# Kernel optimization log

Hardware: AMD Instinct MI355X
Metric: run time of the kernel (lower is better)

The kernel has to match this reference:

```python
import jax, jax.numpy as jnp
import numpy as np

N_NODES = 50000
N_EDGES = 800000
D = 128
N_RELS = 460  # 2 * num_rels
N_BASES = 32
SUBMAT = D // N_BASES  # 4
INV_TEMP = 0.1


def setup_inputs() -> dict:
    key = jax.random.key(0)
    ks = jax.random.split(key, 16)
    return {
        "h": jax.random.normal(ks[0], (N_NODES, D), jnp.float32),
        "first_prev": jax.random.normal(ks[1], (N_NODES, D), jnp.float32),
        "second_prev": jax.random.normal(ks[2], (N_NODES, D), jnp.float32),
        "time_diff": jax.random.uniform(ks[3], (N_NODES, 1), jnp.float32),
        "edge_src": jax.random.randint(ks[4], (N_EDGES,), 0, N_NODES, jnp.int32),
        "edge_dst": jax.random.randint(ks[5], (N_EDGES,), 0, N_NODES, jnp.int32),
        "edge_type": jax.random.randint(ks[6], (N_EDGES,), 0, N_RELS, jnp.int32),
        "edge_norm": jax.random.uniform(ks[7], (N_EDGES, 1), jnp.float32),
        "node_norm": jax.random.uniform(ks[8], (N_NODES, 1), jnp.float32),
        "W1": jax.random.normal(ks[9], (N_RELS, N_BASES * SUBMAT * SUBMAT), jnp.float32) * 0.05,
        "W2": jax.random.normal(ks[10], (N_RELS, N_BASES * SUBMAT * SUBMAT), jnp.float32) * 0.05,
        "loop_w1": jax.random.normal(ks[11], (D, D), jnp.float32) * 0.05,
        "loop_w2": jax.random.normal(ks[12], (D, D), jnp.float32) * 0.05,
        "time_w1": jax.random.normal(ks[13], (D, D), jnp.float32) * 0.05,
        "time_w2": jax.random.normal(ks[14], (D, D), jnp.float32) * 0.05,
    }


def _drgcn_layer(h, prev, time_diff, W, loop_w, time_w,
                 edge_src, edge_dst, edge_type, edge_norm, node_norm, activate):
    n = h.shape[0]
    # self-loop message (dropout is identity in eval)
    loop_msg = h @ loop_w                                     # [N, D]
    # block-diagonal per-edge message: gather relation blocks + batched small matmul
    w = W[edge_type].reshape(-1, N_BASES, SUBMAT, SUBMAT)     # [E, B, si, so]
    hs = h[edge_src].reshape(-1, N_BASES, SUBMAT)             # [E, B, si]
    msg = jnp.einsum('ebi,ebio->ebo', hs, w).reshape(-1, h.shape[1])  # [E, D]
    msg = msg * edge_norm                                     # per-edge norm
    agg = jax.ops.segment_sum(msg, edge_dst, num_segments=n)  # scatter-sum to dst
    agg = agg * node_norm                                     # apply_func node norm
    # time-decay residual + self-loop (bias=None in this config)
    out = agg + (prev @ time_w) * jnp.exp(-time_diff * INV_TEMP) + loop_msg
    if activate:
        out = jax.nn.relu(out)
    return out


def reference(h, first_prev, second_prev, time_diff,
              edge_src, edge_dst, edge_type, edge_norm, node_norm,
              W1, W2, loop_w1, loop_w2, time_w1, time_w2):
    h1 = _drgcn_layer(h, first_prev, time_diff, W1, loop_w1, time_w1,
                      edge_src, edge_dst, edge_type, edge_norm, node_norm, activate=False)
    h2 = _drgcn_layer(h1, second_prev, time_diff, W2, loop_w2, time_w2,
                      edge_src, edge_dst, edge_type, edge_norm, node_norm, activate=True)
    return (h1, h2)
```

## Files before the change

### kernel.cpp

```cpp
#include <hip/hip_runtime.h>

#define NN 50000
#define NE 800000
#define DD 128
#define NPAD 50176
#define NBLK_SCAN 196

typedef __attribute__((ext_vector_type(8))) short short8;
typedef __attribute__((ext_vector_type(4))) float f32x4;

static __device__ __forceinline__ float b2f(unsigned short u) {
    return __builtin_bit_cast(float, (unsigned)u << 16);
}
static __device__ __forceinline__ float b2f_lo(unsigned u) {
    return __builtin_bit_cast(float, u << 16);
}
static __device__ __forceinline__ float b2f_hi(unsigned u) {
    return __builtin_bit_cast(float, u & 0xffff0000u);
}
static __device__ __forceinline__ unsigned short f2b(float f) {
    unsigned u = __builtin_bit_cast(unsigned, f);
    u += 0x7FFFu + ((u >> 16) & 1u);
    return (unsigned short)(u >> 16);
}

__global__ __launch_bounds__(256) void k_hist(
    const int* __restrict__ edst, int* __restrict__ cnt)
{
    const int e = blockIdx.x * 256 + threadIdx.x;
    atomicAdd(&cnt[edst[e]], 1);
}

__global__ __launch_bounds__(256) void k_scan_a(
    const int* __restrict__ cnt, int* __restrict__ bsum)
{
    __shared__ int s[256];
    const int t = threadIdx.x;
    s[t] = cnt[blockIdx.x * 256 + t];
    __syncthreads();
    for (int d = 128; d > 0; d >>= 1) {
        if (t < d) s[t] += s[t + d];
        __syncthreads();
    }
    if (t == 0) bsum[blockIdx.x] = s[0];
}

__global__ __launch_bounds__(256) void k_scan_b(int* __restrict__ bsum)
{
    __shared__ int s[256];
    const int t = threadIdx.x;
    s[t] = (t < NBLK_SCAN) ? bsum[t] : 0;
    __syncthreads();
    for (int d = 1; d < 256; d <<= 1) {
        int v = (t >= d) ? s[t - d] : 0;
        __syncthreads();
        s[t] += v;
        __syncthreads();
    }
    bsum[t] = (t == 0) ? 0 : s[t - 1];
}

__global__ __launch_bounds__(256) void k_scan_c(
    const int* __restrict__ cnt, const int* __restrict__ bsum,
    int* __restrict__ off, int* __restrict__ cur)
{
    __shared__ int s[256];
    const int t = threadIdx.x;
    const int i = blockIdx.x * 256 + t;
    const int c = cnt[i];
    s[t] = c;
    __syncthreads();
    for (int d = 1; d < 256; d <<= 1) {
        int v = (t >= d) ? s[t - d] : 0;
        __syncthreads();
        s[t] += v;
        __syncthreads();
    }
    const int ex = bsum[blockIdx.x] + s[t] - c;
    off[i] = ex;
    cur[i] = ex;
}

__global__ __launch_bounds__(256) void k_scatter(
    const int* __restrict__ esrc, const int* __restrict__ edst,
    const int* __restrict__ etyp, const float* __restrict__ enorm,
    int* __restrict__ cur, int4* __restrict__ sedge)
{
    const int e = blockIdx.x * 256 + threadIdx.x;
    const int d = edst[e];
    const int pos = atomicAdd(&cur[d], 1);
    sedge[pos] = make_int4(esrc[e], etyp[e],
                           __builtin_bit_cast(int, enorm[e]), d);
}

__global__ __launch_bounds__(256) void conv_x(
    const float* __restrict__ x, const float* __restrict__ fprev,
    const float* __restrict__ sprev, const float* __restrict__ tdiff,
    unsigned short* __restrict__ X1, unsigned short* __restrict__ X2)
{
    const int idx = blockIdx.x * 256 + threadIdx.x;
    const int n = idx >> 7, j = idx & 127;
    const float d = __expf(-tdiff[n] * 0.1f);
    X1[(size_t)n * 256 + j]       = f2b(x[(size_t)n * 128 + j]);
    X1[(size_t)n * 256 + 128 + j] = f2b(fprev[(size_t)n * 128 + j] * d);
    X2[(size_t)n * 256 + 128 + j] = f2b(sprev[(size_t)n * 128 + j] * d);
}

__global__ __launch_bounds__(256) void k_wprep(
    const float* __restrict__ W1, const float* __restrict__ W2,
    unsigned short* __restrict__ W1b, unsigned short* __restrict__ W2b,
    const float* __restrict__ lw1, const float* __restrict__ tw1,
    const float* __restrict__ lw2, const float* __restrict__ tw2,
    unsigned short* __restrict__ Wp1, unsigned short* __restrict__ Wp2)
{
    const int gb = blockIdx.x;
    if (gb < 1840) {
        const int i = gb * 256 + threadIdx.x;
        if (i < 460 * 512) W1b[i] = f2b(W1[i]);
        else               W2b[i - 460 * 512] = f2b(W2[i - 460 * 512]);
    } else {
        const int g = (gb - 1840) * 256 + threadIdx.x;
        const int c = g & 4095;
        const float* lw = (g < 4096) ? lw1 : lw2;
        const float* tw = (g < 4096) ? tw1 : tw2;
        unsigned short* Wp = (g < 4096) ? Wp1 : Wp2;
        const int ct = c >> 9, ks = (c >> 6) & 7, lane = c & 63;
        const int col = ct * 16 + (lane & 15);
        unsigned short* o = Wp + (size_t)c * 8;
        #pragma unroll
        for (int i = 0; i < 8; ++i) {
            const int k = ks * 32 + (lane >> 4) * 8 + i;
            const float v = (k < 128) ? lw[(size_t)k * 128 + col]
                                      : tw[(size_t)(k - 128) * 128 + col];
            o[i] = f2b(v);
        }
    }
}

__device__ __forceinline__ void agg_edge(
    const unsigned short* __restrict__ x,
    const unsigned short* __restrict__ Wb,
    const int4* __restrict__ sedge, int i,
    int woff, int l, float4& acc)
{
    const int4 e = sedge[i];
    const int src = __builtin_amdgcn_readfirstlane(e.x);
    const int typ = __builtin_amdgcn_readfirstlane(e.y);
    const float nr = __builtin_bit_cast(float, __builtin_amdgcn_readfirstlane(e.z));
    const unsigned hw = ((const unsigned*)(x + (size_t)src * 256))[l];
    const uint4 wv = *(const uint4*)(Wb + (size_t)typ * 512 + woff);
    const float h0 = b2f_lo(hw) * nr;
    const float h1 = b2f_hi(hw) * nr;
    acc.x += h0 * b2f_lo(wv.x) + h1 * b2f_lo(wv.z);
    acc.y += h0 * b2f_hi(wv.x) + h1 * b2f_hi(wv.z);
    acc.z += h0 * b2f_lo(wv.y) + h1 * b2f_lo(wv.w);
    acc.w += h0 * b2f_hi(wv.y) + h1 * b2f_hi(wv.w);
}

__global__ __launch_bounds__(256) void k_agg2(
    const unsigned short* __restrict__ x,
    const int4*  __restrict__ sedge,
    const int*   __restrict__ off,
    const unsigned short* __restrict__ Wb,
    const float* __restrict__ nnorm,
    float*       __restrict__ agg)
{
    const int l = threadIdx.x & 63;
    const int n = blockIdx.x * 4 + (threadIdx.x >> 6);
    const int beg = off[n], end = off[n + 1];
    const int woff = (l >> 1) * 16 + (l & 1) * 8;

    float4 a0 = {0,0,0,0}, a1 = {0,0,0,0}, a2 = {0,0,0,0}, a3 = {0,0,0,0};

    int i = beg;
    for (; i + 4 <= end; i += 4) {
        agg_edge(x, Wb, sedge, i,     woff, l, a0);
        agg_edge(x, Wb, sedge, i + 1, woff, l, a1);
        agg_edge(x, Wb, sedge, i + 2, woff, l, a2);
        agg_edge(x, Wb, sedge, i + 3, woff, l, a3);
    }
    for (; i < end; ++i) agg_edge(x, Wb, sedge, i, woff, l, a0);

    float4 s;
    s.x = (a0.x + a1.x) + (a2.x + a3.x);
    s.y = (a0.y + a1.y) + (a2.y + a3.y);
    s.z = (a0.z + a1.z) + (a2.z + a3.z);
    s.w = (a0.w + a1.w) + (a2.w + a3.w);
    s.x += __shfl_xor(s.x, 1);
    s.y += __shfl_xor(s.y, 1);
    s.z += __shfl_xor(s.z, 1);
    s.w += __shfl_xor(s.w, 1);

    const float nn = nnorm[n];
    const float e0 = (l & 1) ? s.z : s.x;
    const float e1 = (l & 1) ? s.w : s.y;
    float2* outp = (float2*)(agg + (size_t)n * DD + (l >> 1) * 4 + (l & 1) * 2);
    *outp = make_float2(e0 * nn, e1 * nn);
}

template<int ACT, int WRITE_NEXT>
__global__ __launch_bounds__(256) void combine_mfma(
    const float* __restrict__ agg,
    const unsigned short* __restrict__ X,
    const unsigned short* __restrict__ Wp,
    float* __restrict__ out,
    unsigned short* __restrict__ Xnext)
{
    const int t = threadIdx.x;
    const int l = t & 63;
    const int w = t >> 6;
    const int wr = w >> 1, wc = w & 1;
    const int l15 = l & 15, lhi = l >> 4;
    const int rowbase = blockIdx.x * 64 + wr * 32;

    f32x4 acc[2][4] = {};

    const int ar0 = min(rowbase + l15, NN - 1);
    const int ar1 = min(rowbase + 16 + l15, NN - 1);
    const unsigned short* a0p = X + (size_t)ar0 * 256 + lhi * 8;
    const unsigned short* a1p = X + (size_t)ar1 * 256 + lhi * 8;
    const unsigned short* bp  = Wp + (size_t)(wc * 4) * 8 * 512 + (size_t)l * 8;

    #pragma unroll
    for (int ks = 0; ks < 8; ++ks) {
        const short8 a0 = *(const short8*)(a0p + ks * 32);
        const short8 a1 = *(const short8*)(a1p + ks * 32);
        #pragma unroll
        for (int ct = 0; ct < 4; ++ct) {
            const short8 b = *(const short8*)(bp + (size_t)(ct * 8 + ks) * 512);
            acc[0][ct] = __builtin_amdgcn_mfma_f32_16x16x32_bf16(a0, b, acc[0][ct], 0, 0, 0);
            acc[1][ct] = __builtin_amdgcn_mfma_f32_16x16x32_bf16(a1, b, acc[1][ct], 0, 0, 0);
        }
    }

    __shared__ float cs[64][132];
    #pragma unroll
    for (int rg = 0; rg < 2; ++rg)
        #pragma unroll
        for (int ct = 0; ct < 4; ++ct)
            #pragma unroll
            for (int q = 0; q < 4; ++q)
                cs[wr * 32 + rg * 16 + lhi * 4 + q][wc * 64 + ct * 16 + l15]
                    = acc[rg][ct][q];
    __syncthreads();

    const int r = t >> 2;
    const int s = t & 3;
    const int grow = blockIdx.x * 64 + r;
    if (grow < NN) {
        const float* aggr = agg + (size_t)grow * DD;
        float*       outr = out + (size_t)grow * DD;
        #pragma unroll
        for (int i = 0; i < 8; ++i) {
            const int c = s * 4 + i * 16;
            const float4 a  = *(const float4*)(aggr + c);
            const float4 cc = *(const float4*)&cs[r][c];
            float4 v = make_float4(a.x + cc.x, a.y + cc.y, a.z + cc.z, a.w + cc.w);
            if (ACT) {
                v.x = fmaxf(v.x, 0.f); v.y = fmaxf(v.y, 0.f);
                v.z = fmaxf(v.z, 0.f); v.w = fmaxf(v.w, 0.f);
            }
            *(float4*)(outr + c) = v;
            if (WRITE_NEXT) {
                ushort4 u;
                u.x = f2b(v.x); u.y = f2b(v.y); u.z = f2b(v.z); u.w = f2b(v.w);
                *(ushort4*)(Xnext + (size_t)grow * 256 + c) = u;
            }
        }
    }
}

__device__ __forceinline__ float pick4(float4 v, int o) {
    float a = (o & 1) ? v.y : v.x;
    float b = (o & 1) ? v.w : v.z;
    return (o & 2) ? b : a;
}

__global__ __launch_bounds__(256) void k_agg_t2(
    const float* __restrict__ x, const int4* __restrict__ sedge,
    const int* __restrict__ off, const float* __restrict__ W,
    float* __restrict__ agg)
{
    const int lane = threadIdx.x & 63;
    const int n    = blockIdx.x * 4 + (threadIdx.x >> 6);
    const int beg = off[n], end = off[n + 1];
    float4 acca = make_float4(0.f, 0.f, 0.f, 0.f);
    float4 accb = make_float4(0.f, 0.f, 0.f, 0.f);
    for (int i = beg; i < end; ++i) {
        const int4 e = sedge[i];
        const float nr = __builtin_bit_cast(float, e.z);
        const float* wr = W + (size_t)e.y * 512 + 4 * lane;
        const float4 wa = *(const float4*)wr;
        const float4 wb = *(const float4*)(wr + 256);
        const float* hr = x + (size_t)e.x * DD;
        const float ha = hr[lane] * nr;
        const float hb = hr[64 + lane] * nr;
        acca.x += ha * wa.x; acca.y += ha * wa.y; acca.z += ha * wa.z; acca.w += ha * wa.w;
        accb.x += hb * wb.x; accb.y += hb * wb.y; accb.z += hb * wb.z; accb.w += hb * wb.w;
    }
    #pragma unroll
    for (int d = 1; d <= 2; d <<= 1) {
        acca.x += __shfl_xor(acca.x, d); acca.y += __shfl_xor(acca.y, d);
        acca.z += __shfl_xor(acca.z, d); acca.w += __shfl_xor(acca.w, d);
        accb.x += __shfl_xor(accb.x, d); accb.y += __shfl_xor(accb.y, d);
        accb.z += __shfl_xor(accb.z, d); accb.w += __shfl_xor(accb.w, d);
    }
    const int o = lane & 3;
    agg[(size_t)n * DD + lane]      = pick4(acca, o);
    agg[(size_t)n * DD + 64 + lane] = pick4(accb, o);
}

__global__ __launch_bounds__(256) void edge_msg(
    const float* __restrict__ x, const int* __restrict__ esrc,
    const int* __restrict__ edst, const int* __restrict__ etyp,
    const float* __restrict__ enorm, const float* __restrict__ W,
    float* __restrict__ agg)
{
    const int t  = threadIdx.x;
    const int le = t >> 7;
    const int j  = t & 127;
    const int e  = blockIdx.x * 2 + le;
    __shared__ float sh[2][DD];
    sh[le][j] = x[(size_t)esrc[e] * DD + j];
    __syncthreads();
    const int b = j >> 2, o = j & 3;
    const float* wr = W + (size_t)etyp[e] * 512 + b * 16 + o;
    const float4 hv = *(const float4*)&sh[le][b * 4];
    float m = hv.x * wr[0] + hv.y * wr[4] + hv.z * wr[8] + hv.w * wr[12];
    m *= enorm[e];
    atomicAdd(&agg[(size_t)edst[e] * DD + j], m);
}

template<int ACT>
__global__ __launch_bounds__(256) void combine(
    float* __restrict__ out, const float* __restrict__ x,
    const float* __restrict__ prev, const float* __restrict__ tdiff,
    const float* __restrict__ nnorm, const float* __restrict__ lw,
    const float* __restrict__ tw)
{
    const int t = threadIdx.x;
    const int j = t & 127;
    const int r = t >> 7;
    const int base = blockIdx.x * 8;
    __shared__ float sh[8][DD];
    __shared__ float sp[8][DD];
    #pragma unroll
    for (int q = 0; q < 4; ++q) {
        const int m = q * 2 + r;
        const int n = base + m;
        const float decay = __expf(-tdiff[n] * 0.1f);
        sh[m][j] = x[(size_t)n * DD + j];
        sp[m][j] = prev[(size_t)n * DD + j] * decay;
    }
    __syncthreads();
    float acc[4] = {0.f, 0.f, 0.f, 0.f};
    for (int k = 0; k < DD; k += 4) {
        float wl[4], wt[4];
        #pragma unroll
        for (int kk = 0; kk < 4; ++kk) {
            wl[kk] = lw[(size_t)(k + kk) * DD + j];
            wt[kk] = tw[(size_t)(k + kk) * DD + j];
        }
        #pragma unroll
        for (int q = 0; q < 4; ++q) {
            const int m = q * 2 + r;
            const float4 a = *(const float4*)&sh[m][k];
            const float4 p = *(const float4*)&sp[m][k];
            acc[q] += a.x * wl[0] + a.y * wl[1] + a.z * wl[2] + a.w * wl[3]
                    + p.x * wt[0] + p.y * wt[1] + p.z * wt[2] + p.w * wt[3];
        }
    }
    #pragma unroll
    for (int q = 0; q < 4; ++q) {
        const int m = q * 2 + r;
        const int n = base + m;
        float v = out[(size_t)n * DD + j] * nnorm[n] + acc[q];
        if (ACT) v = fmaxf(v, 0.f);
        out[(size_t)n * DD + j] = v;
    }
}

extern "C" void kernel_launch(void* const* d_in, const int* in_sizes, int n_in,
                              void* d_out, int out_size, void* d_ws, size_t ws_size,
                              hipStream_t stream) {
    const float* h     = (const float*)d_in[0];
    const float* fprev = (const float*)d_in[1];
    const float* sprev = (const float*)d_in[2];
    const float* tdiff = (const float*)d_in[3];
    const int*   esrc  = (const int*)d_in[4];
    const int*   edst  = (const int*)d_in[5];
    const int*   etyp  = (const int*)d_in[6];
    const float* enorm = (const float*)d_in[7];
    const float* nnorm = (const float*)d_in[8];
    const float* W1    = (const float*)d_in[9];
    const float* W2    = (const float*)d_in[10];
    const float* lw1   = (const float*)d_in[11];
    const float* lw2   = (const float*)d_in[12];
    const float* tw1   = (const float*)d_in[13];
    const float* tw2   = (const float*)d_in[14];

    float* h1 = (float*)d_out;
    float* h2 = h1 + (size_t)NN * DD;
    const size_t layer_bytes = (size_t)NN * DD * sizeof(float);

    char* wsp = (char*)d_ws;
    int*   cnt   = (int*)wsp;  wsp += (size_t)NPAD * 4;
    int*   off   = (int*)wsp;  wsp += (size_t)NPAD * 4;
    int*   cur   = (int*)wsp;  wsp += (size_t)NPAD * 4;
    int*   bsum  = (int*)wsp;  wsp += 256 * 4;
    int4*  sedge = (int4*)wsp; wsp += (size_t)NE * 16;
    const size_t ws_sorted = (size_t)(wsp - (char*)d_ws);
    unsigned short* X1   = (unsigned short*)wsp; wsp += (size_t)NN * 256 * 2;
    unsigned short* X2   = (unsigned short*)wsp; wsp += (size_t)NN * 256 * 2;
    unsigned short* Wc1p = (unsigned short*)wsp; wsp += 4096 * 8 * 2;
    unsigned short* Wc2p = (unsigned short*)wsp; wsp += 4096 * 8 * 2;
    unsigned short* W1b  = (unsigned short*)wsp; wsp += (size_t)460 * 512 * 2;
    unsigned short* W2b  = (unsigned short*)wsp; wsp += (size_t)460 * 512 * 2;
    const size_t ws_full = (size_t)(wsp - (char*)d_ws);

    const int grid_mm = (NN + 63) / 64;

    if (ws_size >= ws_full) {
        hipMemsetAsync(cnt, 0, (size_t)NPAD * 4, stream);
        k_hist   <<<NE / 256, 256, 0, stream>>>(edst, cnt);
        k_scan_a <<<NBLK_SCAN, 256, 0, stream>>>(cnt, bsum);
        k_scan_b <<<1, 256, 0, stream>>>(bsum);
        k_scan_c <<<NBLK_SCAN, 256, 0, stream>>>(cnt, bsum, off, cur);
        k_scatter<<<NE / 256, 256, 0, stream>>>(esrc, edst, etyp, enorm, cur, sedge);
        conv_x <<<NN * DD / 256, 256, 0, stream>>>(h, fprev, sprev, tdiff, X1, X2);
        k_wprep<<<1872, 256, 0, stream>>>(W1, W2, W1b, W2b,
                                          lw1, tw1, lw2, tw2, Wc1p, Wc2p);
        k_agg2<<<NN / 4, 256, 0, stream>>>(X1, sedge, off, W1b, nnorm, h1);
        combine_mfma<0, 1><<<grid_mm, 256, 0, stream>>>(h1, X1, Wc1p, h1, X2);
        k_agg2<<<NN / 4, 256, 0, stream>>>(X2, sedge, off, W2b, nnorm, h2);
        combine_mfma<1, 0><<<grid_mm, 256, 0, stream>>>(h2, X2, Wc2p, h2, nullptr);
    } else if (ws_size >= ws_sorted) {
        hipMemsetAsync(cnt, 0, (size_t)NPAD * 4, stream);
        k_hist   <<<NE / 256, 256, 0, stream>>>(edst, cnt);
        k_scan_a <<<NBLK_SCAN, 256, 0, stream>>>(cnt, bsum);
        k_scan_b <<<1, 256, 0, stream>>>(bsum);
        k_scan_c <<<NBLK_SCAN, 256, 0, stream>>>(cnt, bsum, off, cur);
        k_scatter<<<NE / 256, 256, 0, stream>>>(esrc, edst, etyp, enorm, cur, sedge);
        k_agg_t2<<<NN / 4, 256, 0, stream>>>(h, sedge, off, W1, h1);
        combine<0><<<NN / 8, 256, 0, stream>>>(h1, h, fprev, tdiff, nnorm, lw1, tw1);
        k_agg_t2<<<NN / 4, 256, 0, stream>>>(h1, sedge, off, W2, h2);
        combine<1><<<NN / 8, 256, 0, stream>>>(h2, h1, sprev, tdiff, nnorm, lw2, tw2);
    } else {
        hipMemsetAsync(h1, 0, layer_bytes, stream);
        edge_msg<<<NE / 2, 256, 0, stream>>>(h, esrc, edst, etyp, enorm, W1, h1);
        combine<0><<<NN / 8, 256, 0, stream>>>(h1, h, fprev, tdiff, nnorm, lw1, tw1);
        hipMemsetAsync(h2, 0, layer_bytes, stream);
        edge_msg<<<NE / 2, 256, 0, stream>>>(h1, esrc, edst, etyp, enorm, W2, h2);
        combine<1><<<NN / 8, 256, 0, stream>>>(h2, h1, sprev, tdiff, nnorm, lw2, tw2);
    }
}
```

Baseline: 430.1 us.

## Fuse edge aggregation with MFMA combine into one kernel per layer

Merges the per-node gather/aggregation kernel and the MFMA self-loop/time-decay combine kernel into a single kernel per layer. Each block of 64 nodes first aggregates neighbour messages into shared memory, with each wave handling 16 nodes in sequence. It then adds that tile to the MFMA results before writing the output and the next layer's bf16 input. This removes the fp32 agg round trip through global memory and two kernel launches. In exchange the grid drops from 12500 small blocks to about 782, which reduces the number of waves available to hide the latency of the gathers.

```diff
diff --git a/kernel.cpp b/kernel.cpp
--- a/kernel.cpp
+++ b/kernel.cpp
@@ -9,9 +9,6 @@
 typedef __attribute__((ext_vector_type(8))) short short8;
 typedef __attribute__((ext_vector_type(4))) float f32x4;
 
-static __device__ __forceinline__ float b2f(unsigned short u) {
-    return __builtin_bit_cast(float, (unsigned)u << 16);
-}
 static __device__ __forceinline__ float b2f_lo(unsigned u) {
     return __builtin_bit_cast(float, u << 16);
 }
@@ -157,61 +154,65 @@
     acc.w += h0 * b2f_hi(wv.y) + h1 * b2f_hi(wv.w);
 }
 
-__global__ __launch_bounds__(256) void k_agg2(
-    const unsigned short* __restrict__ x,
+template<int ACT, int WRITE_NEXT>
+__global__ __launch_bounds__(256) void layer_fused(
+    const unsigned short* __restrict__ X,
     const int4*  __restrict__ sedge,
     const int*   __restrict__ off,
     const unsigned short* __restrict__ Wb,
+    const unsigned short* __restrict__ Wp,
     const float* __restrict__ nnorm,
-    float*       __restrict__ agg)
-{
-    const int l = threadIdx.x & 63;
-    const int n = blockIdx.x * 4 + (threadIdx.x >> 6);
-    const int beg = off[n], end = off[n + 1];
-    const int woff = (l >> 1) * 16 + (l & 1) * 8;
-
-    float4 a0 = {0,0,0,0}, a1 = {0,0,0,0}, a2 = {0,0,0,0}, a3 = {0,0,0,0};
-
-    int i = beg;
-    for (; i + 4 <= end; i += 4) {
-        agg_edge(x, Wb, sedge, i,     woff, l, a0);
-        agg_edge(x, Wb, sedge, i + 1, woff, l, a1);
-        agg_edge(x, Wb, sedge, i + 2, woff, l, a2);
-        agg_edge(x, Wb, sedge, i + 3, woff, l, a3);
-    }
-    for (; i < end; ++i) agg_edge(x, Wb, sedge, i, woff, l, a0);
-
-    float4 s;
-    s.x = (a0.x + a1.x) + (a2.x + a3.x);
-    s.y = (a0.y + a1.y) + (a2.y + a3.y);
-    s.z = (a0.z + a1.z) + (a2.z + a3.z);
-    s.w = (a0.w + a1.w) + (a2.w + a3.w);
-    s.x += __shfl_xor(s.x, 1);
-    s.y += __shfl_xor(s.y, 1);
-    s.z += __shfl_xor(s.z, 1);
-    s.w += __shfl_xor(s.w, 1);
-
-    const float nn = nnorm[n];
-    const float e0 = (l & 1) ? s.z : s.x;
-    const float e1 = (l & 1) ? s.w : s.y;
-    float2* outp = (float2*)(agg + (size_t)n * DD + (l >> 1) * 4 + (l & 1) * 2);
-    *outp = make_float2(e0 * nn, e1 * nn);
-}
-
-template<int ACT, int WRITE_NEXT>
-__global__ __launch_bounds__(256) void combine_mfma(
-    const float* __restrict__ agg,
-    const unsigned short* __restrict__ X,
-    const unsigned short* __restrict__ Wp,
     float* __restrict__ out,
     unsigned short* __restrict__ Xnext)
 {
     const int t = threadIdx.x;
     const int l = t & 63;
     const int w = t >> 6;
+    const int nodebase = blockIdx.x * 64;
+
+    __shared__ float cs[64][132];
+
+    const int woff = (l >> 1) * 16 + (l & 1) * 8;
+    const int cofs = (l >> 1) * 4 + (l & 1) * 2;
+
+    for (int m = 0; m < 16; ++m) {
+        const int ln = w * 16 + m;
+        const int n  = nodebase + ln;
+        if (n < NN) {
+            const int beg = off[n], end = off[n + 1];
+            float4 a0 = {0,0,0,0}, a1 = {0,0,0,0}, a2 = {0,0,0,0}, a3 = {0,0,0,0};
+            int i = beg;
+            for (; i + 4 <= end; i += 4) {
+                agg_edge(X, Wb, sedge, i,     woff, l, a0);
+                agg_edge(X, Wb, sedge, i + 1, woff, l, a1);
+                agg_edge(X, Wb, sedge, i + 2, woff, l, a2);
+                agg_edge(X, Wb, sedge, i + 3, woff, l, a3);
+            }
+            for (; i < end; ++i) agg_edge(X, Wb, sedge, i, woff, l, a0);
+
+            float4 s;
+            s.x = (a0.x + a1.x) + (a2.x + a3.x);
+            s.y = (a0.y + a1.y) + (a2.y + a3.y);
+            s.z = (a0.z + a1.z) + (a2.z + a3.z);
+            s.w = (a0.w + a1.w) + (a2.w + a3.w);
+            s.x += __shfl_xor(s.x, 1);
+            s.y += __shfl_xor(s.y, 1);
+            s.z += __shfl_xor(s.z, 1);
+            s.w += __shfl_xor(s.w, 1);
+
+            const float nn = nnorm[n];
+            const float e0 = ((l & 1) ? s.z : s.x) * nn;
+            const float e1 = ((l & 1) ? s.w : s.y) * nn;
+            *(float2*)&cs[ln][cofs] = make_float2(e0, e1);
+        } else {
+            *(float2*)&cs[ln][cofs] = make_float2(0.f, 0.f);
+        }
+    }
+    __syncthreads();
+
     const int wr = w >> 1, wc = w & 1;
     const int l15 = l & 15, lhi = l >> 4;
-    const int rowbase = blockIdx.x * 64 + wr * 32;
+    const int rowbase = nodebase + wr * 32;
 
     f32x4 acc[2][4] = {};
 
@@ -233,7 +234,16 @@
         }
     }
 
-    __shared__ float cs[64][132];
+    #pragma unroll
+    for (int rg = 0; rg < 2; ++rg)
+        #pragma unroll
+        for (int ct = 0; ct < 4; ++ct)
+            #pragma unroll
+            for (int q = 0; q < 4; ++q)
+                acc[rg][ct][q] += cs[wr * 32 + rg * 16 + lhi * 4 + q]
+                                    [wc * 64 + ct * 16 + l15];
+    __syncthreads();
+
     #pragma unroll
     for (int rg = 0; rg < 2; ++rg)
         #pragma unroll
@@ -246,16 +256,13 @@
 
     const int r = t >> 2;
     const int s = t & 3;
-    const int grow = blockIdx.x * 64 + r;
+    const int grow = nodebase + r;
     if (grow < NN) {
-        const float* aggr = agg + (size_t)grow * DD;
-        float*       outr = out + (size_t)grow * DD;
+        float* outr = out + (size_t)grow * DD;
         #pragma unroll
         for (int i = 0; i < 8; ++i) {
             const int c = s * 4 + i * 16;
-            const float4 a  = *(const float4*)(aggr + c);
-            const float4 cc = *(const float4*)&cs[r][c];
-            float4 v = make_float4(a.x + cc.x, a.y + cc.y, a.z + cc.z, a.w + cc.w);
+            float4 v = *(const float4*)&cs[r][c];
             if (ACT) {
                 v.x = fmaxf(v.x, 0.f); v.y = fmaxf(v.y, 0.f);
                 v.z = fmaxf(v.z, 0.f); v.w = fmaxf(v.w, 0.f);
@@ -430,10 +437,10 @@
         conv_x <<<NN * DD / 256, 256, 0, stream>>>(h, fprev, sprev, tdiff, X1, X2);
         k_wprep<<<1872, 256, 0, stream>>>(W1, W2, W1b, W2b,
                                           lw1, tw1, lw2, tw2, Wc1p, Wc2p);
-        k_agg2<<<NN / 4, 256, 0, stream>>>(X1, sedge, off, W1b, nnorm, h1);
-        combine_mfma<0, 1><<<grid_mm, 256, 0, stream>>>(h1, X1, Wc1p, h1, X2);
-        k_agg2<<<NN / 4, 256, 0, stream>>>(X2, sedge, off, W2b, nnorm, h2);
-        combine_mfma<1, 0><<<grid_mm, 256, 0, stream>>>(h2, X2, Wc2p, h2, nullptr);
+        layer_fused<0, 1><<<grid_mm, 256, 0, stream>>>(
+            X1, sedge, off, W1b, Wc1p, nnorm, h1, X2);
+        layer_fused<1, 0><<<grid_mm, 256, 0, stream>>>(
+            X2, sedge, off, W2b, Wc2p, nnorm, h2, nullptr);
     } else if (ws_size >= ws_sorted) {
         hipMemsetAsync(cnt, 0, (size_t)NPAD * 4, stream);
         k_hist   <<<NE / 256, 256, 0, stream>>>(edst, cnt);
```

Result: slower. 462.4 us (+7.5%).
